# Performance work log

Hardware: AMD Instinct MI355X
Metric: run time of the kernel (lower is better)

Reference implementation:

```python
import jax, jax.numpy as jnp
import numpy as np

D_MODEL = 1024
D_STATE = 64
D_CONV = 4
EXPAND = 2
HEADDIM = 64  # Hydra default (config.headdim is not forwarded by the block)
D_INNER = EXPAND * D_MODEL            # 2048
NHEADS = D_INNER // HEADDIM           # 32
D_IN_PROJ = 2 * D_INNER + 2 * D_STATE + 2 * NHEADS  # 4288
CONV_DIM = D_INNER + 2 * D_STATE      # 2176
CHUNK = 64
EPS = 1e-5
BATCH, SEQLEN = 4, 2048


def setup_inputs() -> dict:
    key = jax.random.key(0)
    ks = jax.random.split(key, 8)
    w = lambda k, shape, s=0.02: (jax.random.normal(k, shape, jnp.float32) * s)
    dt = jnp.linspace(1e-3, 1e-1, NHEADS, dtype=jnp.float32)
    return {
        "hidden_states": jax.random.normal(ks[0], (BATCH, SEQLEN, D_MODEL), jnp.float32),
        "residual": jax.random.normal(ks[1], (BATCH, SEQLEN, D_MODEL), jnp.float32),
        "norm_weight": jnp.ones((D_MODEL,), jnp.float32),
        "in_proj_w": w(ks[2], (D_IN_PROJ, D_MODEL)),
        "conv_w": w(ks[3], (CONV_DIM, 1, D_CONV), 0.2),
        "conv_b": jnp.zeros((CONV_DIM,), jnp.float32),
        "dt_bias": jnp.log(jnp.expm1(dt)),  # inverse-softplus init, as in Mamba2/Hydra
        "A_log": jnp.log(jnp.linspace(1.0, 16.0, NHEADS, dtype=jnp.float32)),
        "D": jnp.ones((NHEADS,), jnp.float32),
        "fc_D_w": w(ks[4], (NHEADS, D_INNER)),
        "gn_weight": jnp.ones((D_INNER,), jnp.float32),
        "out_proj_w": w(ks[5], (D_MODEL, D_INNER)),
    }


def _rmsnorm(x, weight):
    x = x.astype(jnp.float32)
    return x * jax.lax.rsqrt(jnp.mean(x * x, axis=-1, keepdims=True) + EPS) * weight


def _segsum(x):
    # x: (..., T) -> lower-triangular cumulative segment sums, -inf above diag
    T = x.shape[-1]
    cs = jnp.cumsum(x, axis=-1)
    ss = cs[..., :, None] - cs[..., None, :]
    mask = jnp.tril(jnp.ones((T, T), bool))
    return jnp.where(mask, ss, -jnp.inf)


def _ssd(X, A, Bm, Cm, block):
    # Chunked SSD (mamba_chunk_scan_combined math, D=None, z=None, ngroups=1)
    # X: (b,l,h,p) = dt*x ; A: (b,l,h) = dt*A ; Bm, Cm: (b,l,n)
    b, l, h, p = X.shape
    c = l // block
    X = X.reshape(b, c, block, h, p)
    A = A.reshape(b, c, block, h).transpose(0, 3, 1, 2)          # (b,h,c,l)
    Bm = Bm.reshape(b, c, block, -1)
    Cm = Cm.reshape(b, c, block, -1)
    A_cum = jnp.cumsum(A, axis=-1)
    Lmat = jnp.exp(_segsum(A))                                   # (b,h,c,l,s)
    Y_diag = jnp.einsum("bcln,bcsn,bhcls,bcshp->bclhp", Cm, Bm, Lmat, X)
    decay = jnp.exp(A_cum[..., -1:] - A_cum)                     # (b,h,c,l)
    states = jnp.einsum("bcln,bhcl,bclhp->bchpn", Bm, decay, X)
    states = jnp.concatenate([jnp.zeros_like(states[:, :1]), states], axis=1)
    dchunk = jnp.exp(_segsum(jnp.pad(A_cum[..., -1], ((0, 0), (0, 0), (1, 0)))))
    states = jnp.einsum("bhzc,bchpn->bzhpn", dchunk, states)[:, :-1]
    Y_off = jnp.einsum("bcln,bchpn,bhcl->bclhp", Cm, states, jnp.exp(A_cum))
    return (Y_diag + Y_off).reshape(b, l, h, p)


def _hydra(h, in_proj_w, conv_w, conv_b, dt_bias, A_log, D, fc_D_w, gn_weight, out_proj_w):
    b, l, _ = h.shape
    zxbcdt = h @ in_proj_w.T                                     # (b,l,4288)
    z = zxbcdt[..., :D_INNER]
    xBC = zxbcdt[..., D_INNER:D_INNER + CONV_DIM]
    dt = zxbcdt[..., D_INNER + CONV_DIM:]                        # (b,l,2H)
    # fwd heads + time-flipped bwd heads, stacked on batch -> (2b,l,H)
    dt = jnp.concatenate([dt[..., :NHEADS], jnp.flip(dt[..., NHEADS:], axis=1)], axis=0)
    dt = jax.nn.softplus(dt + dt_bias)
    A = -jnp.exp(A_log)                                          # (H,)
    # causal depthwise conv, kernel D_CONV
    pad = jnp.pad(xBC, ((0, 0), (D_CONV - 1, 0), (0, 0)))
    conv = conv_b + sum(pad[:, k:k + l, :] * conv_w[:, 0, k] for k in range(D_CONV))
    xBC = jax.nn.silu(conv)
    x = xBC[..., :D_INNER]
    Bm = xBC[..., D_INNER:D_INNER + D_STATE]
    Cm = xBC[..., D_INNER + D_STATE:]
    x2 = jnp.concatenate([x, jnp.flip(x, axis=1)], axis=0)       # (2b,l,d_inner)
    B2 = jnp.concatenate([Bm, jnp.flip(Bm, axis=1)], axis=0)
    C2 = jnp.concatenate([Cm, jnp.flip(Cm, axis=1)], axis=0)
    X = x2.reshape(2 * b, l, NHEADS, HEADDIM) * dt[..., None]    # dt-discretized input
    y = _ssd(X, dt * A, B2, C2, CHUNK).reshape(2 * b, l, D_INNER)
    # quasiseparable combine: strict lower (shift fwd by +1) + strict upper + data-dep diag
    y = jnp.roll(y, 1, axis=1).at[:, 0, :].set(0.0)
    y = y[:b] + jnp.flip(y[b:], axis=1)
    Deff = x @ fc_D_w.T + D                                      # (b,l,H)
    y = y + x * jnp.repeat(Deff, HEADDIM, axis=-1)
    y = _rmsnorm(y * jax.nn.silu(z), gn_weight)                  # gated RMSNorm
    return y @ out_proj_w.T


def reference(hidden_states, residual, norm_weight, in_proj_w, conv_w, conv_b,
              dt_bias, A_log, D, fc_D_w, gn_weight, out_proj_w):
    res = (hidden_states + residual).astype(jnp.float32)         # residual_in_fp32
    h = _rmsnorm(res, norm_weight)                               # fused add+RMSNorm (prenorm)
    out = _hydra(h, in_proj_w, conv_w, conv_b, dt_bias, A_log, D, fc_D_w, gn_weight, out_proj_w)
    return out, res
```

## Files before the change

kernel.cpp:

```cpp
#include <hip/hip_runtime.h>

typedef __attribute__((ext_vector_type(4))) float f32x4;
typedef __attribute__((ext_vector_type(8))) short short8;
typedef __attribute__((ext_vector_type(8))) unsigned short ushort8;
typedef unsigned short u16;
typedef unsigned int u32;

#define DMODEL 1024
#define DINNER 2048
#define NH     32
#define DIP    4288
#define DIP_PAD 4352
#define CONVD  2176
#define LSEQ   2048
#define ROWS   8192
#define NCHUNK 32

static __device__ __forceinline__ float bf2f(u16 u) {
  u32 x = ((u32)u) << 16;
  return __builtin_bit_cast(float, x);
}
static __device__ __forceinline__ u16 f2bf(float f) {
  u32 x = __builtin_bit_cast(u32, f);
  x += 0x7fffu + ((x >> 16) & 1u);
  return (u16)(x >> 16);
}
static __device__ __forceinline__ f32x4 mfma16(short8 a, short8 b, f32x4 c) {
  return __builtin_amdgcn_mfma_f32_16x16x32_bf16(a, b, c, 0, 0, 0);
}

#define GLDS(gp, lp)                                                     \
  __builtin_amdgcn_global_load_lds(                                     \
      (const __attribute__((address_space(1))) void*)(gp),              \
      (__attribute__((address_space(3))) void*)(lp), 16, 0, 0)

__global__ __launch_bounds__(256) void k_cast(const float* __restrict__ s, u16* __restrict__ d) {
  size_t i = ((size_t)blockIdx.x * 256 + threadIdx.x) * 4;
  float4 v = *(const float4*)(s + i);
  u32 lo = (u32)f2bf(v.x) | ((u32)f2bf(v.y) << 16);
  u32 hi = (u32)f2bf(v.z) | ((u32)f2bf(v.w) << 16);
  *(uint2*)(d + i) = make_uint2(lo, hi);
}

__global__ __launch_bounds__(256) void k_addnorm(const float* __restrict__ h,
                                                 const float* __restrict__ r,
                                                 const float* __restrict__ nw,
                                                 float* __restrict__ res,
                                                 u16* __restrict__ hn) {
  int row = blockIdx.x, t = threadIdx.x;
  const float4* hp = (const float4*)(h + (size_t)row * DMODEL);
  const float4* rp = (const float4*)(r + (size_t)row * DMODEL);
  float4 a = hp[t], b = rp[t];
  float4 s;
  s.x = a.x + b.x; s.y = a.y + b.y; s.z = a.z + b.z; s.w = a.w + b.w;
  ((float4*)(res + (size_t)row * DMODEL))[t] = s;
  float ss = s.x * s.x + s.y * s.y + s.z * s.z + s.w * s.w;
  for (int m = 32; m; m >>= 1) ss += __shfl_xor(ss, m);
  __shared__ float wsum[4];
  if ((t & 63) == 0) wsum[t >> 6] = ss;
  __syncthreads();
  float tot = wsum[0] + wsum[1] + wsum[2] + wsum[3];
  float rinv = rsqrtf(tot * (1.0f / DMODEL) + 1e-5f);
  float4 w4 = ((const float4*)nw)[t];
  u32 lo = (u32)f2bf(s.x * rinv * w4.x) | ((u32)f2bf(s.y * rinv * w4.y) << 16);
  u32 hi = (u32)f2bf(s.z * rinv * w4.z) | ((u32)f2bf(s.w * rinv * w4.w) << 16);
  *(uint2*)(hn + (size_t)row * DMODEL + t * 4) = make_uint2(lo, hi);
}

template <int MODE>
__global__ __launch_bounds__(512) void k_gemm(const u16* __restrict__ A,
                                              const u16* __restrict__ Bw, int K, int nN,
                                              float* __restrict__ outf,
                                              u16* __restrict__ zb, u16* __restrict__ xb,
                                              float* __restrict__ dtp,
                                              const float* __restrict__ dt_bias) {
  constexpr int ABY = 128 * 64 * 2;
  constexpr int BBY = 256 * 64 * 2;
  constexpr int TB = ABY + BBY;
  __shared__ char lds[2 * TB];

  const int tid = threadIdx.x, wave = tid >> 6, lane = tid & 63;
  const int wm = wave >> 2, wn = wave & 3;
  const int lr = lane & 15, lg = lane >> 4;

  const int cpx = gridDim.x >> 3;
  const int orig = blockIdx.x;
  const int wg = (orig & 7) * cpx + (orig >> 3);
  const int brow = (wg / nN) * 128;
  const int bcol = (wg % nN) * 256;
  const int NK = K >> 6;

  size_t srcA[2], srcB[4];
#pragma unroll
  for (int g = 0; g < 2; ++g) {
    int d = g * 8192 + tid * 16;
    int s = d ^ (((d >> 7) & 7) << 4);
    srcA[g] = (size_t)(brow + (s >> 7)) * K + ((s & 127) >> 1);
  }
#pragma unroll
  for (int g = 0; g < 4; ++g) {
    int d = g * 8192 + tid * 16;
    int s = d ^ (((d >> 7) & 7) << 4);
    srcB[g] = (size_t)(bcol + (s >> 7)) * K + ((s & 127) >> 1);
  }

  auto STAGE = [&](int buf, int kt) {
    char* base = lds + buf * TB;
    size_t koff = (size_t)kt * 64;
#pragma unroll
    for (int g = 0; g < 2; ++g)
      GLDS(A + srcA[g] + koff, base + g * 8192 + wave * 1024);
#pragma unroll
    for (int g = 0; g < 4; ++g)
      GLDS(Bw + srcB[g] + koff, base + ABY + g * 8192 + wave * 1024);
  };

  int offA[4][2], offB[4][2];
#pragma unroll
  for (int i = 0; i < 4; ++i)
#pragma unroll
    for (int ks = 0; ks < 2; ++ks) {
      int rA = wm * 64 + i * 16 + lr;
      offA[i][ks] = (rA * 128 + ks * 64 + lg * 16) ^ ((lr & 7) << 4);
      int rB = wn * 64 + i * 16 + lr;
      offB[i][ks] = ABY + ((rB * 128 + ks * 64 + lg * 16) ^ ((lr & 7) << 4));
    }

  f32x4 acc[4][4] = {};
  STAGE(0, 0);
  asm volatile("s_waitcnt vmcnt(0)" ::: "memory");
  __builtin_amdgcn_s_barrier();
  for (int t = 0; t < NK; ++t) {
    const int cur = t & 1;
    if (t + 1 < NK) STAGE(cur ^ 1, t + 1);
    const char* bb = lds + cur * TB;
    short8 af[4], bfr[4];
#pragma unroll
    for (int i = 0; i < 4; ++i) af[i] = *(const short8*)(bb + offA[i][0]);
#pragma unroll
    for (int j = 0; j < 4; ++j) bfr[j] = *(const short8*)(bb + offB[j][0]);
    __builtin_amdgcn_s_setprio(1);
#pragma unroll
    for (int i = 0; i < 4; ++i)
#pragma unroll
      for (int j = 0; j < 4; ++j) acc[i][j] = mfma16(af[i], bfr[j], acc[i][j]);
    __builtin_amdgcn_s_setprio(0);
#pragma unroll
    for (int i = 0; i < 4; ++i) af[i] = *(const short8*)(bb + offA[i][1]);
#pragma unroll
    for (int j = 0; j < 4; ++j) bfr[j] = *(const short8*)(bb + offB[j][1]);
    __builtin_amdgcn_s_setprio(1);
#pragma unroll
    for (int i = 0; i < 4; ++i)
#pragma unroll
      for (int j = 0; j < 4; ++j) acc[i][j] = mfma16(af[i], bfr[j], acc[i][j]);
    __builtin_amdgcn_s_setprio(0);
    if (t + 1 < NK) {
      asm volatile("s_waitcnt vmcnt(0)" ::: "memory");
      __builtin_amdgcn_s_barrier();
    }
  }

  const int mb = brow + wm * 64 + lg * 4;
  const int nb = bcol + wn * 64 + lr;
#pragma unroll
  for (int i = 0; i < 4; ++i)
#pragma unroll
    for (int j = 0; j < 4; ++j)
#pragma unroll
      for (int rr = 0; rr < 4; ++rr) {
        int m = mb + i * 16 + rr;
        int n = nb + j * 16;
        float v = acc[i][j][rr];
        if constexpr (MODE == 1) {
          outf[(size_t)m * 1024 + n] = v;
        } else {
          if (n < DINNER) {
            zb[(size_t)m * DINNER + n] = f2bf(v);
          } else if (n < DINNER + CONVD) {
            xb[(size_t)m * CONVD + (n - DINNER)] = f2bf(v);
          } else if (n < DIP) {
            int h2 = n - (DINNER + CONVD);
            float uu = v + dt_bias[h2 & 31];
            float sp = (uu > 20.f) ? uu : log1pf(expf(uu));
            int bb2 = m >> 11, tt = m & 2047;
            int obb = bb2, ot = tt;
            if (h2 >= 32) { obb = bb2 + 4; ot = 2047 - tt; }
            dtp[((size_t)(obb << 11) + ot) * NH + (h2 & 31)] = sp;
          }
        }
      }
}

__global__ __launch_bounds__(256) void k_conv(const u16* __restrict__ xbc,
                                              const float* __restrict__ cw,
                                              const float* __restrict__ cb,
                                              u16* __restrict__ xc, u16* __restrict__ bm,
                                              u16* __restrict__ cm) {
  int e = blockIdx.x * 256 + threadIdx.x;
  int c8 = e % 272;
  int r = e / 272;
  int c = c8 * 8;
  int b = r >> 11, t = r & 2047;
  float4 w[8];
  float a[8];
#pragma unroll
  for (int j = 0; j < 8; ++j) {
    w[j] = *(const float4*)&cw[(c + j) * 4];
    a[j] = cb[c + j];
  }
  const u16* base = xbc + (size_t)(b << 11) * CONVD + c;
#pragma unroll
  for (int k = 0; k < 4; ++k) {
    int tt = t - 3 + k;
    if (tt >= 0) {
      ushort8 v = *(const ushort8*)(base + (size_t)tt * CONVD);
#pragma unroll
      for (int j = 0; j < 8; ++j) a[j] += bf2f(v[j]) * ((const float*)&w[j])[k];
    }
  }
  ushort8 o;
#pragma unroll
  for (int j = 0; j < 8; ++j) {
    float s = a[j] * (1.f / (1.f + expf(-a[j])));
    o[j] = f2bf(s);
  }
  if (c8 < 256) *(ushort8*)(xc + (size_t)r * DINNER + c) = o;
  else if (c8 < 264) *(ushort8*)(bm + (size_t)r * 64 + (c - DINNER)) = o;
  else *(ushort8*)(cm + (size_t)r * 64 + (c - DINNER - 64)) = o;
}

__global__ __launch_bounds__(512) void k_ssd(const u16* __restrict__ xc,
                                             const u16* __restrict__ bmat,
                                             const u16* __restrict__ cmat,
                                             const float* __restrict__ dtp,
                                             const float* __restrict__ alog,
                                             u16* __restrict__ y0, u16* __restrict__ y1) {
  const int h = blockIdx.x & 31;
  const int grp = blockIdx.x >> 5;
  const int dir = grp >> 2;
  const int bt = grp & 3;
  const int tid = threadIdx.x, wave = tid >> 6, lane = tid & 63;
  const int lq = wave >> 1, wh = wave & 1;
  const int lr = lane & 15, lg = lane >> 4;
  const float Ah = -expf(alog[h]);

  __shared__ u16 sB[64][72];
  __shared__ u16 sC[64][72];
  __shared__ u16 sXM[64][72];
  __shared__ u16 sXT[64][72];
  __shared__ u16 sBT[64][72];
  __shared__ u16 sSb[64][72];
  __shared__ float sS[64][68];
  __shared__ float sAc[64], sEA[64], sSc[64], sDt[64];

  for (int i = tid; i < 64 * 64; i += 512) {
    sS[i >> 6][i & 63] = 0.f;
    sSb[i >> 6][i & 63] = 0;
  }

  const int srow = tid >> 3, q8 = (tid & 7) * 8;

  auto rowOf = [&](int c) {
    int tdir = c * 64 + srow;
    return bt * LSEQ + (dir ? (LSEQ - 1 - tdir) : tdir);
  };

  int rg = rowOf(0);
  ushort8 rB = *(const ushort8*)(bmat + (size_t)rg * 64 + q8);
  ushort8 rC = *(const ushort8*)(cmat + (size_t)rg * 64 + q8);
  ushort8 rX = *(const ushort8*)(xc + (size_t)rg * DINNER + h * 64 + q8);

  for (int c = 0; c < NCHUNK; ++c) {
    *(ushort8*)&sB[srow][q8] = rB;
    *(ushort8*)&sC[srow][q8] = rC;
    *(ushort8*)&sXM[srow][q8] = rX;
    __syncthreads();

    {
      ushort8 vx, vb;
#pragma unroll
      for (int i = 0; i < 8; ++i) {
        vx[i] = sXM[wave * 8 + i][lane];
        vb[i] = sB[wave * 8 + i][lane];
      }
      *(ushort8*)&sXT[lane][wave * 8] = vx;
      *(ushort8*)&sBT[lane][wave * 8] = vb;
    }
    if (wave == 0) {
      int s = lane;
      float dv = dtp[((size_t)grp * LSEQ + c * 64 + s) * NH + h];
      float a = dv * Ah;
      float x = a;
#pragma unroll
      for (int d = 1; d < 64; d <<= 1) {
        float y = __shfl_up(x, d);
        if (s >= d) x += y;
      }
      float tot = __shfl(x, 63);
      sAc[s] = x;
      sEA[s] = expf(x);
      sSc[s] = expf(tot - x) * dv;
      sDt[s] = dv;
    }
    __syncthreads();

    if (c + 1 < NCHUNK) {
      int rg2 = rowOf(c + 1);
      rB = *(const ushort8*)(bmat + (size_t)rg2 * 64 + q8);
      rC = *(const ushort8*)(cmat + (size_t)rg2 * 64 + q8);
      rX = *(const ushort8*)(xc + (size_t)rg2 * DINNER + h * 64 + q8);
    }

    f32x4 acc_y[2] = {};
    {
      f32x4 acc_g[2] = {};
#pragma unroll
      for (int ks = 0; ks < 2; ++ks) {
        int kof = ks * 32 + lg * 8;
        short8 af = *(const short8*)&sC[lq * 16 + lr][kof];
#pragma unroll
        for (int nt = 0; nt < 2; ++nt) {
          short8 bf = *(const short8*)&sB[wh * 32 + nt * 16 + lr][kof];
          acc_g[nt] = mfma16(af, bf, acc_g[nt]);
        }
      }
#pragma unroll
      for (int ks = 0; ks < 2; ++ks) {
        int kof = ks * 32 + lg * 8;
        short8 af = *(const short8*)&sC[lq * 16 + lr][kof];
#pragma unroll
        for (int nt = 0; nt < 2; ++nt) {
          short8 bf = *(const short8*)&sSb[wh * 32 + nt * 16 + lr][kof];
          acc_y[nt] = mfma16(af, bf, acc_y[nt]);
        }
      }
#pragma unroll
      for (int nt = 0; nt < 2; ++nt)
#pragma unroll
        for (int rr = 0; rr < 4; ++rr) {
          int l = lq * 16 + lg * 4 + rr;
          int s = wh * 32 + nt * 16 + lr;
          float g = acc_g[nt][rr];
          float m = (l >= s) ? g * sDt[s] * expf(sAc[l] - sAc[s]) : 0.f;
          sXM[l][s] = f2bf(m);
        }
    }
    __syncthreads();

#pragma unroll
    for (int nt = 0; nt < 2; ++nt)
#pragma unroll
      for (int rr = 0; rr < 4; ++rr) acc_y[nt][rr] *= sEA[lq * 16 + lg * 4 + rr];
#pragma unroll
    for (int ks = 0; ks < 2; ++ks) {
      int kof = ks * 32 + lg * 8;
      short8 af = *(const short8*)&sXM[lq * 16 + lr][kof];
#pragma unroll
      for (int nt = 0; nt < 2; ++nt) {
        short8 bf = *(const short8*)&sXT[wh * 32 + nt * 16 + lr][kof];
        acc_y[nt] = mfma16(af, bf, acc_y[nt]);
      }
    }
#pragma unroll
    for (int nt = 0; nt < 2; ++nt)
#pragma unroll
      for (int rr = 0; rr < 4; ++rr) {
        int l = lq * 16 + lg * 4 + rr;
        int p = wh * 32 + nt * 16 + lr;
        int tg = c * 64 + l;
        if (tg <= LSEQ - 2) {
          float v = acc_y[nt][rr];
          if (dir == 0)
            y0[((size_t)bt * LSEQ + tg + 1) * DINNER + h * 64 + p] = f2bf(v);
          else
            y1[((size_t)bt * LSEQ + (LSEQ - 2 - tg)) * DINNER + h * 64 + p] = f2bf(v);
        }
      }
    if (c == 0 && tid < 64) {
      if (dir == 0)
        y0[((size_t)bt * LSEQ) * DINNER + h * 64 + tid] = 0;
      else
        y1[((size_t)bt * LSEQ + (LSEQ - 1)) * DINNER + h * 64 + tid] = 0;
    }
    {
      f32x4 acc_s[2] = {};
#pragma unroll
      for (int ks = 0; ks < 2; ++ks) {
        int kof = ks * 32 + lg * 8;
        ushort8 xr = *(const ushort8*)&sXT[lq * 16 + lr][kof];
        short8 af;
#pragma unroll
        for (int e = 0; e < 8; ++e) af[e] = (short)f2bf(bf2f(xr[e]) * sSc[kof + e]);
#pragma unroll
        for (int nt = 0; nt < 2; ++nt) {
          short8 bf = *(const short8*)&sBT[wh * 32 + nt * 16 + lr][kof];
          acc_s[nt] = mfma16(af, bf, acc_s[nt]);
        }
      }
      float lam = sEA[63];
#pragma unroll
      for (int nt = 0; nt < 2; ++nt)
#pragma unroll
        for (int rr = 0; rr < 4; ++rr) {
          int p = lq * 16 + lg * 4 + rr;
          int n = wh * 32 + nt * 16 + lr;
          float ns = lam * sS[p][n] + acc_s[nt][rr];
          sS[p][n] = ns;
          sSb[p][n] = f2bf(ns);
        }
    }
    __syncthreads();
  }
}

__global__ __launch_bounds__(256) void k_deff(const u16* __restrict__ xcv,
                                              const u16* __restrict__ fwb,
                                              const float* __restrict__ Dv,
                                              float* __restrict__ deff) {
  __shared__ float red[2][64][8];
  const int tid = threadIdx.x, wave = tid >> 6, lane = tid & 63;
  const int lr = lane & 15, lg = lane >> 4;
  const int rowg = wave & 1;
  const int kg = wave >> 1;
  const int rb = blockIdx.x * 32 + rowg * 16;
  const u16* xrow = xcv + (size_t)(rb + lr) * DINNER + kg * 1024 + lg * 8;
  const u16* f0 = fwb + (size_t)lr * DINNER + kg * 1024 + lg * 8;
  const u16* f1 = fwb + (size_t)(16 + lr) * DINNER + kg * 1024 + lg * 8;
  f32x4 a0 = {}, a1 = {};
  for (int k = 0; k < 1024; k += 32) {
    short8 bf = *(const short8*)(xrow + k);
    short8 af0 = *(const short8*)(f0 + k);
    short8 af1 = *(const short8*)(f1 + k);
    a0 = mfma16(af0, bf, a0);
    a1 = mfma16(af1, bf, a1);
  }
  if (kg == 1) {
#pragma unroll
    for (int rr = 0; rr < 4; ++rr) {
      red[rowg][lane][rr] = a0[rr];
      red[rowg][lane][4 + rr] = a1[rr];
    }
  }
  __syncthreads();
  if (kg == 0) {
    float4 o0, o1;
#pragma unroll
    for (int rr = 0; rr < 4; ++rr) {
      ((float*)&o0)[rr] = a0[rr] + red[rowg][lane][rr] + Dv[lg * 4 + rr];
      ((float*)&o1)[rr] = a1[rr] + red[rowg][lane][4 + rr] + Dv[16 + lg * 4 + rr];
    }
    *(float4*)&deff[(size_t)(rb + lr) * NH + lg * 4] = o0;
    *(float4*)&deff[(size_t)(rb + lr) * NH + 16 + lg * 4] = o1;
  }
}

__global__ __launch_bounds__(256) void k_gate(const u16* __restrict__ yb0,
                                              const u16* __restrict__ yb1,
                                              const u16* __restrict__ xcv,
                                              const float* __restrict__ deff,
                                              const u16* __restrict__ zb,
                                              const float* __restrict__ gnw,
                                              u16* __restrict__ yn) {
  int row = blockIdx.x, t = threadIdx.x;
  size_t base = (size_t)row * DINNER + t * 8;
  ushort8 y0v = *(const ushort8*)(yb0 + base);
  ushort8 y1v = *(const ushort8*)(yb1 + base);
  ushort8 xv = *(const ushort8*)(xcv + base);
  ushort8 zv = *(const ushort8*)(zb + base);
  float de = deff[row * NH + (t >> 3)];
  float g[8];
  float ss = 0.f;
#pragma unroll
  for (int j = 0; j < 8; ++j) {
    float y = bf2f(y0v[j]) + bf2f(y1v[j]) + bf2f(xv[j]) * de;
    float z = bf2f(zv[j]);
    float gg = y * (z / (1.f + expf(-z)));
    g[j] = gg;
    ss += gg * gg;
  }
  for (int m = 32; m; m >>= 1) ss += __shfl_xor(ss, m);
  __shared__ float wsum[4];
  if ((t & 63) == 0) wsum[t >> 6] = ss;
  __syncthreads();
  float tot = wsum[0] + wsum[1] + wsum[2] + wsum[3];
  float rinv = rsqrtf(tot * (1.0f / DINNER) + 1e-5f);
  u32 w0 = (u32)f2bf(g[0] * rinv * gnw[t * 8 + 0]) | ((u32)f2bf(g[1] * rinv * gnw[t * 8 + 1]) << 16);
  u32 w1 = (u32)f2bf(g[2] * rinv * gnw[t * 8 + 2]) | ((u32)f2bf(g[3] * rinv * gnw[t * 8 + 3]) << 16);
  u32 w2 = (u32)f2bf(g[4] * rinv * gnw[t * 8 + 4]) | ((u32)f2bf(g[5] * rinv * gnw[t * 8 + 5]) << 16);
  u32 w3 = (u32)f2bf(g[6] * rinv * gnw[t * 8 + 6]) | ((u32)f2bf(g[7] * rinv * gnw[t * 8 + 7]) << 16);
  *(uint4*)(yn + base) = make_uint4(w0, w1, w2, w3);
}

extern "C" void kernel_launch(void* const* d_in, const int* in_sizes, int n_in,
                              void* d_out, int out_size, void* d_ws, size_t ws_size,
                              hipStream_t stream) {
  (void)in_sizes; (void)n_in; (void)out_size; (void)ws_size;
  const float* hid = (const float*)d_in[0];
  const float* resin = (const float*)d_in[1];
  const float* nw = (const float*)d_in[2];
  const float* w1 = (const float*)d_in[3];
  const float* cw = (const float*)d_in[4];
  const float* cb = (const float*)d_in[5];
  const float* dtb = (const float*)d_in[6];
  const float* alog = (const float*)d_in[7];
  const float* Dv = (const float*)d_in[8];
  const float* fcw = (const float*)d_in[9];
  const float* gnw = (const float*)d_in[10];
  const float* w2 = (const float*)d_in[11];
  float* out = (float*)d_out;
  float* resout = out + (size_t)ROWS * DMODEL;

  char* ws = (char*)d_ws;
  size_t o = 0;
  auto alloc = [&](size_t bytes) {
    char* p = ws + o;
    o += (bytes + 255) & ~(size_t)255;
    return p;
  };
  u16* W1b = (u16*)alloc((size_t)DIP_PAD * DMODEL * 2);
  u16* HN = (u16*)alloc((size_t)ROWS * DMODEL * 2);
  u16* XBC = (u16*)alloc((size_t)ROWS * CONVD * 2);
  u16* ZB = (u16*)alloc((size_t)ROWS * DINNER * 2);
  u16* XC = (u16*)alloc((size_t)ROWS * DINNER * 2);
  u16* BM = (u16*)alloc((size_t)ROWS * 64 * 2);
  u16* CM = (u16*)alloc((size_t)ROWS * 64 * 2);
  float* DT = (float*)alloc((size_t)8 * LSEQ * NH * 4);
  float* DE = (float*)alloc((size_t)ROWS * NH * 4);
  u16* FWB = (u16*)alloc((size_t)NH * DINNER * 2);
  u16* YB0 = XBC;
  u16* YB1 = (u16*)out;
  u16* W2b = W1b;
  u16* YN = HN;

  k_cast<<<(DIP * DMODEL) / 1024, 256, 0, stream>>>(w1, W1b);
  k_addnorm<<<ROWS, 256, 0, stream>>>(hid, resin, nw, resout, HN);
  k_gemm<0><<<64 * 17, 512, 0, stream>>>(HN, W1b, DMODEL, 17, nullptr, ZB, XBC, DT, dtb);
  k_conv<<<(ROWS * 272) / 256, 256, 0, stream>>>(XBC, cw, cb, XC, BM, CM);
  k_ssd<<<256, 512, 0, stream>>>(XC, BM, CM, DT, alog, YB0, YB1);
  k_cast<<<(DMODEL * DINNER) / 1024, 256, 0, stream>>>(w2, W2b);
  k_cast<<<(NH * DINNER) / 1024, 256, 0, stream>>>(fcw, FWB);
  k_deff<<<ROWS / 32, 256, 0, stream>>>(XC, FWB, Dv, DE);
  k_gate<<<ROWS, 256, 0, stream>>>(YB0, YB1, XC, DE, ZB, gnw, YN);
  k_gemm<1><<<64 * 4, 512, 0, stream>>>(YN, W2b, DINNER, 4, out, nullptr, nullptr, nullptr,
                                        nullptr);
}
```

Baseline: 448.4 us.

## Triple-buffer GEMM LDS pipeline and remap tiles per XCD for L2 reuse

The in_proj/out_proj GEMM now uses three LDS stages instead of two, prefetching two K-tiles ahead and waiting with partial vmcnt counts rather than draining all loads each iteration. All fragments for both k-substeps are read before a second barrier, then the MFMAs run. Workgroup-to-tile mapping is changed so each XCD owns a contiguous band of row tiles, grouped in 8x4 supertiles to improve L2 locality. In exchange LDS use rises by half, which may lower occupancy, and an extra barrier is added per iteration.

```diff
diff --git a/kernel.cpp b/kernel.cpp
--- a/kernel.cpp
+++ b/kernel.cpp
@@ -77,17 +77,27 @@
   constexpr int ABY = 128 * 64 * 2;
   constexpr int BBY = 256 * 64 * 2;
   constexpr int TB = ABY + BBY;
-  __shared__ char lds[2 * TB];
+  __shared__ char lds[3 * TB];
 
   const int tid = threadIdx.x, wave = tid >> 6, lane = tid & 63;
   const int wm = wave >> 2, wn = wave & 3;
   const int lr = lane & 15, lg = lane >> 4;
 
-  const int cpx = gridDim.x >> 3;
-  const int orig = blockIdx.x;
-  const int wg = (orig & 7) * cpx + (orig >> 3);
-  const int brow = (wg / nN) * 128;
-  const int bcol = (wg % nN) * 256;
+  const int xcd = blockIdx.x & 7;
+  const int l = blockIdx.x >> 3;
+  const int nstFull = nN >> 2;
+  int brl, bc;
+  if (l < (nstFull << 5)) {
+    int st = l >> 5, off = l & 31;
+    brl = off & 7;
+    bc = (st << 2) + (off >> 3);
+  } else {
+    int rem = l - (nstFull << 5);
+    brl = rem & 7;
+    bc = (nstFull << 2) + (rem >> 3);
+  }
+  const int brow = (xcd * 8 + brl) * 128;
+  const int bcol = bc * 256;
   const int NK = K >> 6;
 
   size_t srcA[2], srcB[4];
@@ -128,37 +138,46 @@
 
   f32x4 acc[4][4] = {};
   STAGE(0, 0);
-  asm volatile("s_waitcnt vmcnt(0)" ::: "memory");
-  __builtin_amdgcn_s_barrier();
+  STAGE(1, 1);
+  int cur = 0;
   for (int t = 0; t < NK; ++t) {
-    const int cur = t & 1;
-    if (t + 1 < NK) STAGE(cur ^ 1, t + 1);
+    if (t + 2 < NK) {
+      int nb = cur + 2;
+      if (nb >= 3) nb -= 3;
+      STAGE(nb, t + 2);
+      asm volatile("s_waitcnt vmcnt(12)" ::: "memory");
+    } else if (t + 1 < NK) {
+      asm volatile("s_waitcnt vmcnt(6)" ::: "memory");
+    } else {
+      asm volatile("s_waitcnt vmcnt(0)" ::: "memory");
+    }
+    __builtin_amdgcn_sched_barrier(0);
+    __builtin_amdgcn_s_barrier();
+    __builtin_amdgcn_sched_barrier(0);
     const char* bb = lds + cur * TB;
-    short8 af[4], bfr[4];
-#pragma unroll
-    for (int i = 0; i < 4; ++i) af[i] = *(const short8*)(bb + offA[i][0]);
-#pragma unroll
-    for (int j = 0; j < 4; ++j) bfr[j] = *(const short8*)(bb + offB[j][0]);
+    short8 af[4][2], bfr[4][2];
+#pragma unroll
+    for (int i = 0; i < 4; ++i)
+#pragma unroll
+      for (int ks = 0; ks < 2; ++ks) {
+        af[i][ks] = *(const short8*)(bb + offA[i][ks]);
+        bfr[i][ks] = *(const short8*)(bb + offB[i][ks]);
+      }
+    asm volatile("s_waitcnt lgkmcnt(0)" ::: "memory");
+    __builtin_amdgcn_sched_barrier(0);
+    __builtin_amdgcn_s_barrier();
+    __builtin_amdgcn_sched_barrier(0);
     __builtin_amdgcn_s_setprio(1);
 #pragma unroll
-    for (int i = 0; i < 4; ++i)
-#pragma unroll
-      for (int j = 0; j < 4; ++j) acc[i][j] = mfma16(af[i], bfr[j], acc[i][j]);
+    for (int ks = 0; ks < 2; ++ks)
+#pragma unroll
+      for (int i = 0; i < 4; ++i)
+#pragma unroll
+        for (int j = 0; j < 4; ++j) acc[i][j] = mfma16(af[i][ks], bfr[j][ks], acc[i][j]);
     __builtin_amdgcn_s_setprio(0);
-#pragma unroll
-    for (int i = 0; i < 4; ++i) af[i] = *(const short8*)(bb + offA[i][1]);
-#pragma unroll
-    for (int j = 0; j < 4; ++j) bfr[j] = *(const short8*)(bb + offB[j][1]);
-    __builtin_amdgcn_s_setprio(1);
-#pragma unroll
-    for (int i = 0; i < 4; ++i)
-#pragma unroll
-      for (int j = 0; j < 4; ++j) acc[i][j] = mfma16(af[i], bfr[j], acc[i][j]);
-    __builtin_amdgcn_s_setprio(0);
-    if (t + 1 < NK) {
-      asm volatile("s_waitcnt vmcnt(0)" ::: "memory");
-      __builtin_amdgcn_s_barrier();
-    }
+    __builtin_amdgcn_sched_barrier(0);
+    cur = cur + 1;
+    if (cur >= 3) cur = 0;
   }
 
   const int mb = brow + wm * 64 + lg * 4;
```

Measured after the change: 506.7 us. 13.0% more time.
